# Performance work log

Measured on AMD Instinct MI355X. Metric: run time of the kernel, lower is better.

## Reference

```python
import jax, jax.numpy as jnp
import numpy as np

BS, N = 4, 4096
C_IN, C_DSSP, C_HID, NB = 384, 64, 128, 4


def setup_inputs() -> dict:
    key = jax.random.key(0)
    ks = jax.random.split(key, 12)
    sc = lambda k, sh, fan: jax.random.normal(k, sh, jnp.float32) / np.sqrt(fan)
    return {
        "s": jax.random.normal(ks[0], (BS, N, C_IN), jnp.float32),
        "s_initial": jax.random.normal(ks[1], (BS, N, C_IN), jnp.float32),
        "dssp": jax.random.normal(ks[2], (BS, N, C_DSSP), jnp.float32),
        "W_in": sc(ks[3], (C_HID, C_IN), C_IN), "b_in": jnp.zeros((C_HID,), jnp.float32),
        "W_init": sc(ks[4], (C_HID, C_IN), C_IN), "b_init": jnp.zeros((C_HID,), jnp.float32),
        "W_dssp": sc(ks[5], (C_HID, C_DSSP), C_DSSP), "b_dssp": jnp.zeros((C_HID,), jnp.float32),
        "W1": sc(ks[6], (NB, C_HID, C_HID), C_HID), "b1": jnp.zeros((NB, C_HID), jnp.float32),
        "W2": sc(ks[7], (NB, C_HID, C_HID), C_HID), "b2": jnp.zeros((NB, C_HID), jnp.float32),
        "W_out": sc(ks[8], (5, C_HID), C_HID), "b_out": jnp.zeros((5,), jnp.float32),
        "W_mult": sc(ks[9], (2, C_HID), C_HID), "b_mult": jnp.zeros((2,), jnp.float32),
        "scaling_modifier": jnp.float32(0.01),
    }


def reference(s, s_initial, dssp, W_in, b_in, W_init, b_init, W_dssp, b_dssp,
              W1, b1, W2, b2, W_out, b_out, W_mult, b_mult, scaling_modifier):
    relu = jax.nn.relu
    sp = jax.nn.softplus
    lin = lambda x, W, b: jnp.einsum('bnc,hc->bnh', x, W) + b

    h = lin(relu(s), W_in, b_in) + lin(relu(s_initial), W_init, b_init) + lin(relu(dssp), W_dssp, b_dssp)
    for i in range(W1.shape[0]):  # resnet blocks
        h = h + lin(relu(lin(relu(h), W1[i], b1[i])), W2[i], b2[i])
    hr = relu(h)
    corr = lin(hr, W_out, b_out)          # [bs, N, 5]
    mult = lin(hr, W_mult, b_mult)        # [bs, N, 2]
    a, bm = mult[..., 0], mult[..., 1]

    bs, n = corr.shape[0], corr.shape[1]
    idx = jnp.arange(n)
    # diagonal: set corr[...,0], then where(eye) -> sp(diag)*sp(a)+sp(b)
    d0 = sp(corr[..., 0]) * sp(a) + sp(bm)
    # subdiag -1: (i,i-1) += corr[:,i,1]  and  (i+1,i) += corr[:,i,3] (same cells)
    d1 = corr[:, 1:, 1] + corr[:, :-1, 3]
    # subdiag -2: (i,i-2) += corr[:,i,2]  and  (i+2,i) += corr[:,i,4]
    d2 = corr[:, 2:, 2] + corr[:, :-2, 4]

    L = jnp.zeros((bs, n, n), corr.dtype)
    L = L.at[:, idx, idx].set(d0)
    L = L.at[:, idx[1:], idx[:-1]].set(d1)
    L = L.at[:, idx[2:], idx[:-2]].set(d2)
    return scaling_modifier * L  # already lower-banded; tril is identity
```

## Files before the change

### kernel.cpp

```cpp
#include <hip/hip_runtime.h>
#include <math.h>

typedef __bf16 bf16_t;
typedef bf16_t bf16x8 __attribute__((ext_vector_type(8)));
typedef float  floatx4 __attribute__((ext_vector_type(4)));

constexpr int N_SEQ = 4096, BSZ = 4, CIN = 384, CDSSP = 64, CHID = 128, NBLK = 4;
constexpr int NTOK = BSZ * N_SEQ;
constexpr int TOK_PER_BLK = 32;
constexpr int MLP_BLOCKS  = NTOK / TOK_PER_BLK;

constexpr int U_SIN   = 0;
constexpr int U_SINIT = 12288;
constexpr int U_DSSP  = 24576;
constexpr int U_W1    = 26624;
constexpr int U_W2    = 43008;
constexpr int U_END   = 59392;
constexpr int BAND_OFF = U_END * 4;

__device__ __forceinline__ float softplus_f(float x) {
    return fmaxf(x, 0.f) + log1pf(expf(-fabsf(x)));
}
__device__ __forceinline__ unsigned short bf16_bits(bf16_t h) {
    union { bf16_t b; unsigned short u; } c; c.b = h; return c.u;
}
__device__ __forceinline__ bf16_t bits_bf16(unsigned int u) {
    union { unsigned short u; bf16_t b; } c; c.u = (unsigned short)u; return c.b;
}
__device__ __forceinline__ floatx4 mfma16(bf16x8 a, bf16x8 b, floatx4 c) {
    return __builtin_amdgcn_mfma_f32_16x16x32_bf16(a, b, c, 0, 0, 0);
}

__global__ __launch_bounds__(256) void prep_weights(
    const float* __restrict__ Win, const float* __restrict__ Winit,
    const float* __restrict__ Wd,  const float* __restrict__ W1,
    const float* __restrict__ W2,  bf16_t* __restrict__ wsb)
{
    const int t = (int)blockIdx.x * 256 + (int)threadIdx.x;
    const float* src; int K, hi_base, plane, u;
    if (t < 6144)       { src = Win;   K = CIN;   hi_base = U_SIN;   plane = 6144; u = t; }
    else if (t < 12288) { src = Winit; K = CIN;   hi_base = U_SINIT; plane = 6144; u = t - 6144; }
    else if (t < 13312) { src = Wd;    K = CDSSP; hi_base = U_DSSP;  plane = 1024; u = t - 12288; }
    else if (t < 21504) { const int tt = t - 13312, rb = tt >> 11; u = tt & 2047;
                          src = W1 + (size_t)rb * CHID * CHID; K = CHID;
                          hi_base = U_W1 + rb * 4096; plane = 2048; }
    else                { const int tt = t - 21504, rb = tt >> 11; u = tt & 2047;
                          src = W2 + (size_t)rb * CHID * CHID; K = CHID;
                          hi_base = U_W2 + rb * 4096; plane = 2048; }
    const int K8 = K >> 3;
    const int nt = u / (16 * K8);
    const int r  = u - nt * 16 * K8;
    const int kg = r >> 6, r2 = r & 63, c = r2 >> 2, qq = r2 & 3;
    const int j = nt * 16 + c, k8 = kg * 4 + qq;
    const float* sp = src + (size_t)j * K + k8 * 8;
    const float4 a = *(const float4*)sp;
    const float4 b = *(const float4*)(sp + 4);
    const float xs[8] = { a.x, a.y, a.z, a.w, b.x, b.y, b.z, b.w };
    bf16x8 vh, vl;
    #pragma unroll
    for (int i = 0; i < 8; ++i) {
        const float x = xs[i];
        const bf16_t h = (bf16_t)x;
        vh[i] = h; vl[i] = (bf16_t)(x - (float)h);
    }
    *(bf16x8*)(wsb + ((size_t)hi_base + u) * 8)         = vh;
    *(bf16x8*)(wsb + ((size_t)hi_base + plane + u) * 8) = vl;
}

struct BF2 { bf16x8 h[2]; bf16x8 l[2]; };

__device__ __forceinline__ void loadB(const bf16_t* __restrict__ plane, int K8,
                                      int kg, int ntbase, int col, int q, BF2& B) {
    const size_t lo  = (size_t)128 * K8 * 8;
    const size_t nts = (size_t)16 * K8 * 8;
    const bf16_t* base = plane + (size_t)(kg * 64 + col * 4 + q) * 8
                               + (size_t)ntbase * nts;
    #pragma unroll
    for (int nt = 0; nt < 2; ++nt) {
        B.h[nt] = *(const bf16x8*)(base + nt * nts);
        B.l[nt] = *(const bf16x8*)(base + nt * nts + lo);
    }
}

__device__ __forceinline__ void mfma_step(const bf16x8 (&ahi)[2], const bf16x8 (&alo)[2],
                                          const BF2& B, floatx4 (&ac)[2][2]) {
    #pragma unroll
    for (int nt = 0; nt < 2; ++nt)
        #pragma unroll
        for (int mt = 0; mt < 2; ++mt) {
            ac[mt][nt] = mfma16(ahi[mt], B.h[nt], ac[mt][nt]);
            ac[mt][nt] = mfma16(alo[mt], B.h[nt], ac[mt][nt]);
            ac[mt][nt] = mfma16(ahi[mt], B.l[nt], ac[mt][nt]);
        }
}

__device__ __forceinline__ void packXA(const float4 (&X)[2][2],
                                       bf16x8 (&ahi)[2], bf16x8 (&alo)[2]) {
    #pragma unroll
    for (int mt = 0; mt < 2; ++mt) {
        const float xs[8] = { X[mt][0].x, X[mt][0].y, X[mt][0].z, X[mt][0].w,
                              X[mt][1].x, X[mt][1].y, X[mt][1].z, X[mt][1].w };
        #pragma unroll
        for (int i = 0; i < 8; ++i) {
            const float r = fmaxf(xs[i], 0.f);
            const bf16_t h = (bf16_t)r;
            ahi[mt][i] = h;
            alo[mt][i] = (bf16_t)(r - (float)h);
        }
    }
}

__device__ __forceinline__ void ldsA(const uint32_t (*A)[132], int kg, int col, int q,
                                     bf16x8 (&ahi)[2], bf16x8 (&alo)[2]) {
    #pragma unroll
    for (int mt = 0; mt < 2; ++mt) {
        const uint32_t* p = &A[mt * 16 + col][kg * 32 + q * 8];
        const uint4 u0 = *(const uint4*)p;
        const uint4 u1 = *(const uint4*)(p + 4);
        const uint32_t uu[8] = { u0.x, u0.y, u0.z, u0.w, u1.x, u1.y, u1.z, u1.w };
        union { uint32_t u[4]; bf16x8 v; } ch, cl;
        #pragma unroll
        for (int i = 0; i < 4; ++i) {
            ch.u[i] = (uu[2*i] & 0xffffu) | (uu[2*i+1] << 16);
            cl.u[i] = (uu[2*i] >> 16) | (uu[2*i+1] & 0xffff0000u);
        }
        ahi[mt] = ch.v; alo[mt] = cl.v;
    }
}

__device__ __forceinline__ void hidden_pass(const uint32_t (*A)[132],
    const bf16_t* __restrict__ plane, int ntbase, int col, int q, floatx4 (&ac)[2][2])
{
    BF2 B[2];
    loadB(plane, 16, 0, ntbase, col, q, B[0]);
    #pragma unroll 1
    for (int kg = 0; kg < 4; kg += 2) {
        loadB(plane, 16, kg + 1, ntbase, col, q, B[1]);
        bf16x8 ahi[2], alo[2];
        ldsA(A, kg, col, q, ahi, alo);
        mfma_step(ahi, alo, B[0], ac);
        if (kg + 2 < 4) loadB(plane, 16, kg + 2, ntbase, col, q, B[0]);
        ldsA(A, kg + 1, col, q, ahi, alo);
        mfma_step(ahi, alo, B[1], ac);
    }
}

__global__ __launch_bounds__(256) void mlp_kernel(
    const float* __restrict__ s, const float* __restrict__ s_init,
    const float* __restrict__ dssp,
    const float* __restrict__ b_in, const float* __restrict__ b_init,
    const float* __restrict__ b_dssp,
    const float* __restrict__ b1, const float* __restrict__ b2,
    const float* __restrict__ W_out, const float* __restrict__ b_out,
    const float* __restrict__ W_mult, const float* __restrict__ b_mult,
    const bf16_t* __restrict__ wsb, float* __restrict__ band)
{
    __shared__ uint32_t A[32][132];

    const int wid    = (int)threadIdx.x >> 6;
    const int lane   = (int)threadIdx.x & 63;
    const int col    = lane & 15;
    const int q      = lane >> 4;
    const int ntbase = wid * 2;
    const int t0w    = (int)blockIdx.x * TOK_PER_BLK;

    floatx4 hacc[2][2];
    #pragma unroll
    for (int ntl = 0; ntl < 2; ++ntl) {
        const int j = (ntbase + ntl) * 16 + col;
        const float b = b_in[j] + b_init[j] + b_dssp[j];
        floatx4 v = { b, b, b, b };
        hacc[0][ntl] = v; hacc[1][ntl] = v;
    }

    auto loadA = [&](const float* __restrict__ src, int C, int kg, float4 (&X)[2][2]) {
        #pragma unroll
        for (int mt = 0; mt < 2; ++mt) {
            const float* p = src + (size_t)(t0w + mt * 16 + col) * C + kg * 32 + q * 8;
            X[mt][0] = *(const float4*)p;
            X[mt][1] = *(const float4*)(p + 4);
        }
    };

    #pragma unroll 1
    for (int seg = 0; seg < 3; ++seg) {
        const float* src = (seg == 0) ? s : (seg == 1) ? s_init : dssp;
        const int C   = (seg == 2) ? CDSSP : CIN;
        const int NKG = C >> 5;
        const int K8  = C >> 3;
        const bf16_t* plane = wsb +
            (size_t)((seg == 0) ? U_SIN : (seg == 1) ? U_SINIT : U_DSSP) * 8;

        float4 XA[2][2][2];
        BF2 B[2];
        loadA(src, C, 0, XA[0]);
        loadB(plane, K8, 0, ntbase, col, q, B[0]);
        #pragma unroll 1
        for (int kg = 0; kg < NKG; kg += 2) {
            if (kg + 1 < NKG) { loadA(src, C, kg + 1, XA[1]); loadB(plane, K8, kg + 1, ntbase, col, q, B[1]); }
            bf16x8 ahi[2], alo[2];
            packXA(XA[0], ahi, alo);
            mfma_step(ahi, alo, B[0], hacc);
            if (kg + 2 < NKG) { loadA(src, C, kg + 2, XA[0]); loadB(plane, K8, kg + 2, ntbase, col, q, B[0]); }
            if (kg + 1 < NKG) {
                packXA(XA[1], ahi, alo);
                mfma_step(ahi, alo, B[1], hacc);
            }
        }
    }

    auto exchange = [&](floatx4 (&ac)[2][2]) {
        __syncthreads();
        #pragma unroll
        for (int mt = 0; mt < 2; ++mt)
        #pragma unroll
        for (int ntl = 0; ntl < 2; ++ntl)
        #pragma unroll
        for (int r = 0; r < 4; ++r) {
            const float x = fmaxf(ac[mt][ntl][r], 0.f);
            const bf16_t h = (bf16_t)x;
            const bf16_t l = (bf16_t)(x - (float)h);
            A[mt * 16 + q * 4 + r][(ntbase + ntl) * 16 + col] =
                (uint32_t)bf16_bits(h) | ((uint32_t)bf16_bits(l) << 16);
        }
        __syncthreads();
    };

    #pragma unroll 1
    for (int rb = 0; rb < NBLK; ++rb) {
        exchange(hacc);
        floatx4 vacc[2][2];
        #pragma unroll
        for (int ntl = 0; ntl < 2; ++ntl) {
            const float b = b1[rb * CHID + (ntbase + ntl) * 16 + col];
            floatx4 v = { b, b, b, b };
            vacc[0][ntl] = v; vacc[1][ntl] = v;
        }
        hidden_pass(A, wsb + ((size_t)U_W1 + rb * 4096) * 8, ntbase, col, q, vacc);

        exchange(vacc);
        #pragma unroll
        for (int ntl = 0; ntl < 2; ++ntl) {
            const float b = b2[rb * CHID + (ntbase + ntl) * 16 + col];
            #pragma unroll
            for (int mt = 0; mt < 2; ++mt) {
                floatx4 tt = hacc[mt][ntl];
                tt[0] += b; tt[1] += b; tt[2] += b; tt[3] += b;
                hacc[mt][ntl] = tt;
            }
        }
        hidden_pass(A, wsb + ((size_t)U_W2 + rb * 4096) * 8, ntbase, col, q, hacc);
    }
    exchange(hacc);

    const int t    = lane & 31;
    const int half = lane >> 5;
    float d0v, d1v, d2v, d3v;
    const float *w0, *w1, *w2, *w3;
    if (half == 0) {
        w0 = W_out;          w1 = W_out + CHID; w2 = W_out + 2*CHID; w3 = W_out + 3*CHID;
        d0v = b_out[0]; d1v = b_out[1]; d2v = b_out[2]; d3v = b_out[3];
    } else {
        w0 = W_out + 4*CHID; w1 = W_mult;       w2 = W_mult + CHID;  w3 = W_out;
        d0v = b_out[4]; d1v = b_mult[0]; d2v = b_mult[1]; d3v = 0.f;
    }
    #pragma unroll 1
    for (int k = 0; k < CHID; ++k) {
        const uint32_t pk = A[t][k];
        const float x = (float)bits_bf16(pk & 0xffffu) + (float)bits_bf16(pk >> 16);
        d0v = fmaf(x, w0[k], d0v);
        d1v = fmaf(x, w1[k], d1v);
        d2v = fmaf(x, w2[k], d2v);
        d3v = fmaf(x, w3[k], d3v);
    }
    const float av = __shfl(d1v, 32 + t);
    const float bv = __shfl(d2v, 32 + t);
    const int g = t0w + t;
    if (wid == 0 && half == 0) {
        band[g]            = softplus_f(d0v) * softplus_f(av) + softplus_f(bv);
        band[NTOK + g]     = d1v;
        band[2*NTOK + g]   = d2v;
        band[3*NTOK + g]   = d3v;
    } else if (wid == 1 && half == 1) {
        band[4*NTOK + g]   = d0v;
    }
}

__global__ __launch_bounds__(256) void fill_patch(
    const float* __restrict__ band, const float* __restrict__ p_sm,
    float* __restrict__ out)
{
    const int bb = (int)blockIdx.x;
    floatx4* dst = (floatx4*)(out + (size_t)bb * 32768);
    const floatx4 z = { 0.f, 0.f, 0.f, 0.f };
    #pragma unroll 1
    for (int i = (int)threadIdx.x; i < 8192; i += 256)
        __builtin_nontemporal_store(z, dst + i);
    __syncthreads();
    const int r = (int)threadIdx.x;
    if (r < 8) {
        const int g = bb * 8 + r;
        const int b = g >> 12;
        const int i = g & (N_SEQ - 1);
        const float sm = *p_sm;
        const size_t rowbase = (size_t)b * N_SEQ * N_SEQ + (size_t)i * N_SEQ;
        out[rowbase + i] = sm * band[g];
        if (i >= 1) out[rowbase + i - 1] = sm * (band[NTOK + g] + band[3*NTOK + g - 1]);
        if (i >= 2) out[rowbase + i - 2] = sm * (band[2*NTOK + g] + band[4*NTOK + g - 2]);
    }
}

extern "C" void kernel_launch(void* const* d_in, const int* in_sizes, int n_in,
                              void* d_out, int out_size, void* d_ws, size_t ws_size,
                              hipStream_t stream)
{
    const float* s      = (const float*)d_in[0];
    const float* s_init = (const float*)d_in[1];
    const float* dssp   = (const float*)d_in[2];
    const float* W_in   = (const float*)d_in[3];
    const float* b_in   = (const float*)d_in[4];
    const float* W_init = (const float*)d_in[5];
    const float* b_initp= (const float*)d_in[6];
    const float* W_dssp = (const float*)d_in[7];
    const float* b_dsspp= (const float*)d_in[8];
    const float* W1     = (const float*)d_in[9];
    const float* b1     = (const float*)d_in[10];
    const float* W2     = (const float*)d_in[11];
    const float* b2     = (const float*)d_in[12];
    const float* W_out  = (const float*)d_in[13];
    const float* b_out  = (const float*)d_in[14];
    const float* W_mult = (const float*)d_in[15];
    const float* b_mult = (const float*)d_in[16];
    const float* sm     = (const float*)d_in[17];
    bf16_t* wsb  = (bf16_t*)d_ws;
    float*  band = (float*)d_ws + BAND_OFF;
    float*  out  = (float*)d_out;

    prep_weights<<<116, 256, 0, stream>>>(W_in, W_init, W_dssp, W1, W2, wsb);

    mlp_kernel<<<MLP_BLOCKS, 256, 0, stream>>>(
        s, s_init, dssp, b_in, b_initp, b_dsspp, b1, b2,
        W_out, b_out, W_mult, b_mult, (const bf16_t*)wsb, band);

    fill_patch<<<2048, 256, 0, stream>>>(band, sm, out);
}
```

Baseline: 397.3 us.

## Interleave output zero-fill stores into MLP kernel to overlap with compute

Moves the 256 MB zero-fill of the banded output from a separate kernel into the MLP kernel, issuing bursts of nontemporal zero stores between the MFMA phases so memory-bound writes overlap with compute. A slim band_patch kernel then writes only the three diagonals. The exchange barriers are also replaced by an explicit lgkmcnt wait plus s_barrier, so the barrier no longer waits on the outstanding global stores. The risk is that store traffic competes with input loads and the residual zero burst at the end adds tail latency.

```diff
diff --git a/kernel.cpp b/kernel.cpp
--- a/kernel.cpp
+++ b/kernel.cpp
@@ -145,6 +145,12 @@
     }
 }
 
+__device__ __forceinline__ void lds_barrier() {
+    asm volatile("s_waitcnt lgkmcnt(0)" ::: "memory");
+    __builtin_amdgcn_s_barrier();
+    asm volatile("" ::: "memory");
+}
+
 __global__ __launch_bounds__(256) void mlp_kernel(
     const float* __restrict__ s, const float* __restrict__ s_init,
     const float* __restrict__ dssp,
@@ -153,7 +159,8 @@
     const float* __restrict__ b1, const float* __restrict__ b2,
     const float* __restrict__ W_out, const float* __restrict__ b_out,
     const float* __restrict__ W_mult, const float* __restrict__ b_mult,
-    const bf16_t* __restrict__ wsb, float* __restrict__ band)
+    const bf16_t* __restrict__ wsb, float* __restrict__ band,
+    float* __restrict__ out)
 {
     __shared__ uint32_t A[32][132];
 
@@ -163,6 +170,18 @@
     const int q      = lane >> 4;
     const int ntbase = wid * 2;
     const int t0w    = (int)blockIdx.x * TOK_PER_BLK;
+
+    floatx4* zdst = (floatx4*)(out + (size_t)blockIdx.x * (TOK_PER_BLK * N_SEQ));
+    const floatx4 z4 = { 0.f, 0.f, 0.f, 0.f };
+    int zc = 0;
+    auto zburst = [&](int n) {
+        #pragma unroll 1
+        for (int i = 0; i < n; ++i) {
+            if (zc >= 128) break;
+            __builtin_nontemporal_store(z4, zdst + (size_t)zc * 256 + (int)threadIdx.x);
+            ++zc;
+        }
+    };
 
     floatx4 hacc[2][2];
     #pragma unroll
@@ -206,11 +225,12 @@
                 packXA(XA[1], ahi, alo);
                 mfma_step(ahi, alo, B[1], hacc);
             }
+            zburst(6);
         }
     }
 
     auto exchange = [&](floatx4 (&ac)[2][2]) {
-        __syncthreads();
+        lds_barrier();
         #pragma unroll
         for (int mt = 0; mt < 2; ++mt)
         #pragma unroll
@@ -223,12 +243,13 @@
             A[mt * 16 + q * 4 + r][(ntbase + ntl) * 16 + col] =
                 (uint32_t)bf16_bits(h) | ((uint32_t)bf16_bits(l) << 16);
         }
-        __syncthreads();
+        lds_barrier();
     };
 
     #pragma unroll 1
     for (int rb = 0; rb < NBLK; ++rb) {
         exchange(hacc);
+        zburst(3);
         floatx4 vacc[2][2];
         #pragma unroll
         for (int ntl = 0; ntl < 2; ++ntl) {
@@ -237,8 +258,10 @@
             vacc[0][ntl] = v; vacc[1][ntl] = v;
         }
         hidden_pass(A, wsb + ((size_t)U_W1 + rb * 4096) * 8, ntbase, col, q, vacc);
+        zburst(3);
 
         exchange(vacc);
+        zburst(3);
         #pragma unroll
         for (int ntl = 0; ntl < 2; ++ntl) {
             const float b = b2[rb * CHID + (ntbase + ntl) * 16 + col];
@@ -250,8 +273,10 @@
             }
         }
         hidden_pass(A, wsb + ((size_t)U_W2 + rb * 4096) * 8, ntbase, col, q, hacc);
+        zburst(3);
     }
     exchange(hacc);
+    zburst(128);
 
     const int t    = lane & 31;
     const int half = lane >> 5;
@@ -286,28 +311,18 @@
     }
 }
 
-__global__ __launch_bounds__(256) void fill_patch(
+__global__ __launch_bounds__(256) void band_patch(
     const float* __restrict__ band, const float* __restrict__ p_sm,
     float* __restrict__ out)
 {
-    const int bb = (int)blockIdx.x;
-    floatx4* dst = (floatx4*)(out + (size_t)bb * 32768);
-    const floatx4 z = { 0.f, 0.f, 0.f, 0.f };
-    #pragma unroll 1
-    for (int i = (int)threadIdx.x; i < 8192; i += 256)
-        __builtin_nontemporal_store(z, dst + i);
-    __syncthreads();
-    const int r = (int)threadIdx.x;
-    if (r < 8) {
-        const int g = bb * 8 + r;
-        const int b = g >> 12;
-        const int i = g & (N_SEQ - 1);
-        const float sm = *p_sm;
-        const size_t rowbase = (size_t)b * N_SEQ * N_SEQ + (size_t)i * N_SEQ;
-        out[rowbase + i] = sm * band[g];
-        if (i >= 1) out[rowbase + i - 1] = sm * (band[NTOK + g] + band[3*NTOK + g - 1]);
-        if (i >= 2) out[rowbase + i - 2] = sm * (band[2*NTOK + g] + band[4*NTOK + g - 2]);
-    }
+    const int g = (int)blockIdx.x * 256 + (int)threadIdx.x;
+    const int b = g >> 12;
+    const int i = g & (N_SEQ - 1);
+    const float sm = *p_sm;
+    const size_t rowbase = (size_t)b * N_SEQ * N_SEQ + (size_t)i * N_SEQ;
+    out[rowbase + i] = sm * band[g];
+    if (i >= 1) out[rowbase + i - 1] = sm * (band[NTOK + g] + band[3*NTOK + g - 1]);
+    if (i >= 2) out[rowbase + i - 2] = sm * (band[2*NTOK + g] + band[4*NTOK + g - 2]);
 }
 
 extern "C" void kernel_launch(void* const* d_in, const int* in_sizes, int n_in,
@@ -340,7 +355,7 @@
 
     mlp_kernel<<<MLP_BLOCKS, 256, 0, stream>>>(
         s, s_init, dssp, b_in, b_initp, b_dsspp, b1, b2,
-        W_out, b_out, W_mult, b_mult, (const bf16_t*)wsb, band);
-
-    fill_patch<<<2048, 256, 0, stream>>>(band, sm, out);
-}
+        W_out, b_out, W_mult, b_mult, (const bf16_t*)wsb, band, out);
+
+    band_patch<<<NTOK / 256, 256, 0, stream>>>(band, sm, out);
+}
```

New measurement: 394.9 us. Within noise of the previous version (-0.6%).
